# Kernel tuning notes

Hardware: AMD Instinct MI355X
Metric: run time of the kernel (lower is better)

Reference implementation:

```python
import jax, jax.numpy as jnp
import numpy as np

N = 8192
D = 10
T_END = 100


def setup_inputs() -> dict:
    key = jax.random.key(0)
    k_t, k_e, k_mu, k_a, k_b = jax.random.split(key, 5)
    # sorted event times in [0, T)
    time_points = jnp.sort(jax.random.uniform(k_t, (N,), dtype=jnp.float32) * T_END)
    event_types = jax.random.randint(k_e, (N,), 0, D)
    mu = jax.random.normal(k_mu, (D,), dtype=jnp.float32)
    log_alpha = jax.random.normal(k_a, (D, D), dtype=jnp.float32)
    log_beta = jax.random.normal(k_b, (D, D), dtype=jnp.float32)
    return {
        "time_points": time_points,
        "event_types": event_types,
        "mu": mu,
        "log_alpha": log_alpha,
        "log_beta": log_beta,
        "T": T_END,
    }


def reference(time_points, event_types, mu, log_alpha, log_beta, T):
    # transform_params: softplus on raw parameters
    mu_s = jax.nn.softplus(mu)          # (D,)
    alpha = jax.nn.softplus(log_alpha)  # (D, D) receiver x trigger
    beta = jax.nn.softplus(log_beta)    # (D, D)

    n = time_points.shape[0]
    # pairwise causal time differences: dt[i, j] = t_i - t_j
    dt = time_points[:, None] - time_points[None, :]          # (N, N)
    a_mat = alpha[event_types[:, None], event_types[None, :]]  # (N, N)
    b_mat = beta[event_types[:, None], event_types[None, :]]   # (N, N)

    # strict lower-triangular causal mask (j < i)
    mask = jnp.tril(jnp.ones((n, n), dtype=bool), k=-1)
    dt_safe = jnp.where(mask, dt, 0.0)  # avoid exp overflow on masked entries
    interaction = jnp.where(mask, a_mat * b_mat * jnp.exp(-b_mat * dt_safe), 0.0)

    intensities = mu_s[event_types] + jnp.sum(interaction, axis=1)  # (N,)
    positive_ll = jnp.sum(jnp.log(intensities))

    # analytic integral of the intensity over [0, T]
    T_f = jnp.float32(T)
    delta_t = (T_f - time_points)[:, None]          # (N, 1)
    rel_alpha = alpha[:, event_types].T             # (N, D)
    rel_beta = beta[:, event_types].T               # (N, D)
    contributions = rel_alpha * (1.0 - jnp.exp(-rel_beta * delta_t))  # (N, D)
    integral = mu_s * T_f + jnp.sum(contributions, axis=0)            # (D,)

    return positive_ll - jnp.sum(integral)
```

## Files before the change

### kernel.cpp

```cpp
#include <hip/hip_runtime.h>


#define N_EV 8192
#define DT 10
#define LOG2E 1.4426950408889634f
#define TPAD 257

__device__ __forceinline__ float fast_exp2(float x) {
#if __has_builtin(__builtin_amdgcn_exp2f)
    return __builtin_amdgcn_exp2f(x);
#else
    return exp2f(x);
#endif
}

__device__ __forceinline__ float softplus(float x) {
    return fmaxf(x, 0.0f) + log1pf(expf(-fabsf(x)));
}

__device__ __forceinline__ float read_T(const void* p) {
    float f = *(const float*)p;
    if (f > 0.5f && f < 1.0e9f) return f;
    return (float)(*(const int*)p);
}

__global__ __launch_bounds__(256) void hawkes_pairs(
        const float* __restrict__ tp, const int* __restrict__ et,
        const float* __restrict__ la, const float* __restrict__ lb,
        float* __restrict__ partial, float* __restrict__ out) {
    const int ib = blockIdx.y, jb = blockIdx.x;
    if (jb > ib) return;

    __shared__ float  nbl2_s[DT * DT];
    __shared__ float  lab_s[DT * DT];
    __shared__ float2 tile[DT][TPAD];

    const int tid = threadIdx.x;
    if (tid < DT * DT) {
        float a = softplus(la[tid]);
        float b = softplus(lb[tid]);
        nbl2_s[tid] = -b * LOG2E;
        lab_s[tid]  = log2f(a * b);
    }
    __syncthreads();

    const int j0 = jb << 8;
    {
        const float tj = tp[j0 + tid];
        const int   ej = et[j0 + tid];
#pragma unroll
        for (int r = 0; r < DT; ++r) {
            float P = nbl2_s[r * DT + ej];
            float L = fmaf(-P, tj, lab_s[r * DT + ej]);
            tile[r][tid] = make_float2(P, L);
        }
    }
    __syncthreads();

    const int i = (ib << 8) + tid;
    const float ti = tp[i];
    const float2* __restrict__ trow = tile[et[i]];
    const int cnt = (ib == jb) ? tid : 256;

    float a0 = 0.0f, a1 = 0.0f, a2 = 0.0f, a3 = 0.0f;
    int j = 0;
    for (; j + 4 <= cnt; j += 4) {
        float2 c0 = trow[j];
        float2 c1 = trow[j + 1];
        float2 c2 = trow[j + 2];
        float2 c3 = trow[j + 3];
        a0 += fast_exp2(fmaf(c0.x, ti, c0.y));
        a1 += fast_exp2(fmaf(c1.x, ti, c1.y));
        a2 += fast_exp2(fmaf(c2.x, ti, c2.y));
        a3 += fast_exp2(fmaf(c3.x, ti, c3.y));
    }
    for (; j < cnt; ++j) {
        float2 c0 = trow[j];
        a0 += fast_exp2(fmaf(c0.x, ti, c0.y));
    }
    partial[(jb << 13) + i] = (a0 + a1) + (a2 + a3);

    if (ib == 0 && jb == 0 && tid == 0) out[0] = 0.0f;
}

__global__ __launch_bounds__(256) void hawkes_finish(
        const float* __restrict__ tp, const int* __restrict__ et,
        const float* __restrict__ mu, const float* __restrict__ la,
        const float* __restrict__ lb, const void* __restrict__ Tp,
        const float* __restrict__ partial, float* __restrict__ out) {
    __shared__ float mu_s[DT];
    __shared__ float alpha_s[DT * DT];
    __shared__ float nbl2_s[DT * DT];

    const int tid = threadIdx.x;
    if (tid < DT * DT) {
        alpha_s[tid] = softplus(la[tid]);
        nbl2_s[tid]  = -softplus(lb[tid]) * LOG2E;
    }
    if (tid >= 128 && tid < 128 + DT) mu_s[tid - 128] = softplus(mu[tid - 128]);
    __syncthreads();

    const int b = blockIdx.x;
    const int i = (b << 8) + tid;
    const float Tf = read_T(Tp);

    float acc = 0.0f;
    for (int jb = 0; jb <= b; ++jb) acc += partial[(jb << 13) + i];

    const int e = et[i];
    float val = logf(mu_s[e] + acc);

    const float delta = Tf - tp[i];
#pragma unroll
    for (int d = 0; d < DT; ++d)
        val -= alpha_s[d * DT + e] * (1.0f - fast_exp2(nbl2_s[d * DT + e] * delta));

    if (i == 0) {
        float s = 0.0f;
#pragma unroll
        for (int d = 0; d < DT; ++d) s += mu_s[d];
        val -= s * Tf;
    }

    for (int o = 32; o > 0; o >>= 1) val += __shfl_down(val, o);
    __shared__ float wsum[4];
    const int lane = tid & 63, wv = tid >> 6;
    if (lane == 0) wsum[wv] = val;
    __syncthreads();
    if (tid == 0) atomicAdd(out, wsum[0] + wsum[1] + wsum[2] + wsum[3]);
}

extern "C" void kernel_launch(void* const* d_in, const int* in_sizes, int n_in,
                              void* d_out, int out_size, void* d_ws, size_t ws_size,
                              hipStream_t stream) {
    const float* tp = (const float*)d_in[0];
    const int*   et = (const int*)d_in[1];
    const float* mu = (const float*)d_in[2];
    const float* la = (const float*)d_in[3];
    const float* lb = (const float*)d_in[4];
    const void*  Tp = d_in[5];
    float* out = (float*)d_out;
    float* ws  = (float*)d_ws;

    dim3 grid(32, 32);
    hawkes_pairs<<<grid, 256, 0, stream>>>(tp, et, la, lb, ws, out);
    hawkes_finish<<<32, 256, 0, stream>>>(tp, et, mu, la, lb, Tp, ws, out);
}
```

Before: 82.72 us.

## Halve j-chunk width to 128 and read LDS coefficients as float4

The pair kernel now splits the j dimension into 128-wide chunks, so the grid becomes 64x32 and diagonal work is finer-grained, with fewer fully masked lanes. The shared tile is repacked as float4 rows padded to 65 entries, so each load fetches two (P,L) pairs. Per-thread loop counts are clamped from i-j0, and the finish kernel sums twice as many partials. The aim is less idle work on diagonal blocks and better LDS load width, at the cost of more blocks, more partial writes and more reduction reads.

```diff
diff --git a/kernel.cpp b/kernel.cpp
--- a/kernel.cpp
+++ b/kernel.cpp
@@ -4,7 +4,8 @@
 #define N_EV 8192
 #define DT 10
 #define LOG2E 1.4426950408889634f
-#define TPAD 257
+#define JCH 128
+#define R4 65
 
 __device__ __forceinline__ float fast_exp2(float x) {
 #if __has_builtin(__builtin_amdgcn_exp2f)
@@ -29,11 +30,11 @@
         const float* __restrict__ la, const float* __restrict__ lb,
         float* __restrict__ partial, float* __restrict__ out) {
     const int ib = blockIdx.y, jb = blockIdx.x;
-    if (jb > ib) return;
+    if (jb > 2 * ib + 1) return;
 
     __shared__ float  nbl2_s[DT * DT];
     __shared__ float  lab_s[DT * DT];
-    __shared__ float2 tile[DT][TPAD];
+    __shared__ float4 tile4[DT * R4];
 
     const int tid = threadIdx.x;
     if (tid < DT * DT) {
@@ -44,39 +45,41 @@
     }
     __syncthreads();
 
-    const int j0 = jb << 8;
-    {
+    const int j0 = jb * JCH;
+    if (tid < JCH) {
         const float tj = tp[j0 + tid];
         const int   ej = et[j0 + tid];
+        float2* tile2 = (float2*)tile4;
 #pragma unroll
         for (int r = 0; r < DT; ++r) {
             float P = nbl2_s[r * DT + ej];
             float L = fmaf(-P, tj, lab_s[r * DT + ej]);
-            tile[r][tid] = make_float2(P, L);
+            tile2[r * (2 * R4) + tid] = make_float2(P, L);
         }
     }
     __syncthreads();
 
     const int i = (ib << 8) + tid;
     const float ti = tp[i];
-    const float2* __restrict__ trow = tile[et[i]];
-    const int cnt = (ib == jb) ? tid : 256;
+    const float4* __restrict__ row4 = &tile4[et[i] * R4];
+
+    int n = i - j0;
+    n = n < 0 ? 0 : (n > JCH ? JCH : n);
 
     float a0 = 0.0f, a1 = 0.0f, a2 = 0.0f, a3 = 0.0f;
-    int j = 0;
-    for (; j + 4 <= cnt; j += 4) {
-        float2 c0 = trow[j];
-        float2 c1 = trow[j + 1];
-        float2 c2 = trow[j + 2];
-        float2 c3 = trow[j + 3];
+    const int it = n >> 2;
+    for (int k = 0; k < it; ++k) {
+        float4 c0 = row4[2 * k];
+        float4 c1 = row4[2 * k + 1];
         a0 += fast_exp2(fmaf(c0.x, ti, c0.y));
-        a1 += fast_exp2(fmaf(c1.x, ti, c1.y));
-        a2 += fast_exp2(fmaf(c2.x, ti, c2.y));
-        a3 += fast_exp2(fmaf(c3.x, ti, c3.y));
+        a1 += fast_exp2(fmaf(c0.z, ti, c0.w));
+        a2 += fast_exp2(fmaf(c1.x, ti, c1.y));
+        a3 += fast_exp2(fmaf(c1.z, ti, c1.w));
     }
-    for (; j < cnt; ++j) {
-        float2 c0 = trow[j];
-        a0 += fast_exp2(fmaf(c0.x, ti, c0.y));
+    const float2* row2 = (const float2*)row4;
+    for (int j = it << 2; j < n; ++j) {
+        float2 c = row2[j];
+        a0 += fast_exp2(fmaf(c.x, ti, c.y));
     }
     partial[(jb << 13) + i] = (a0 + a1) + (a2 + a3);
 
@@ -105,7 +108,7 @@
     const float Tf = read_T(Tp);
 
     float acc = 0.0f;
-    for (int jb = 0; jb <= b; ++jb) acc += partial[(jb << 13) + i];
+    for (int jb = 0; jb < 2 * b + 2; ++jb) acc += partial[(jb << 13) + i];
 
     const int e = et[i];
     float val = logf(mu_s[e] + acc);
@@ -142,7 +145,7 @@
     float* out = (float*)d_out;
     float* ws  = (float*)d_ws;
 
-    dim3 grid(32, 32);
+    dim3 grid(64, 32);
     hawkes_pairs<<<grid, 256, 0, stream>>>(tp, et, la, lb, ws, out);
     hawkes_finish<<<32, 256, 0, stream>>>(tp, et, mu, la, lb, Tp, ws, out);
 }
```

After: 92.74 us. 1.12x slower.
